# Performance work log

Hardware: AMD Instinct MI355X
Metric: run time of the kernel (lower is better)

Reference implementation:

```python
import jax, jax.numpy as jnp
import numpy as np

BIN_AGG = 16  # binAgg in source
K = 3         # forward-default im2col/col2im kernel size


def _im2col(x, k):
    # torch Im2Col (unfold), pad=0, stride=1, dilation=1
    B, C, H, W = x.shape
    oh, ow = H - k + 1, W - k + 1
    patches = [x[:, :, i:i + oh, j:j + ow] for i in range(k) for j in range(k)]
    cols = jnp.stack(patches, axis=2)            # [B, C, k*k, oh, ow]
    return cols.reshape(B, C * k * k, oh * ow)   # [B, C*k*k, L]


def _col2im(cols, k, H, W):
    # torch Col2Im (fold): overlap-add of patches back to [B, C, H, W]
    B, CK, L = cols.shape
    C = CK // (k * k)
    oh = H - k + 1
    cols = cols.reshape(B, C, k, k, oh, oh)
    img = jnp.zeros((B, C, H, W), cols.dtype)
    for i in range(k):
        for j in range(k):
            img = img.at[:, :, i:i + oh, j:j + oh].add(cols[:, :, i, j])
    return img


def bin_active(x):
    # sign(x) scaled by block-wise mean of |x| over blocks of 16 along last dim
    B, Kd, L = x.shape
    blocks = jnp.abs(x).reshape(B, Kd, L // BIN_AGG, BIN_AGG)
    scale = jnp.mean(blocks, axis=-1, keepdims=True)
    scale = jnp.broadcast_to(scale, blocks.shape).reshape(B, Kd, L)
    return scale * jnp.sign(x)


def setup_inputs() -> dict:
    key = jax.random.key(0)
    ks = jax.random.split(key, 5)
    B, Cin, Cout, H = 8, 64, 128, 130
    x = jax.random.normal(ks[0], (B, Cin, H, H), jnp.float32)
    gamma = 1.0 + 0.1 * jax.random.normal(ks[1], (Cin,), jnp.float32)
    beta = 0.1 * jax.random.normal(ks[2], (Cin,), jnp.float32)
    conv_w = 0.05 * jax.random.normal(ks[3], (Cout, Cin, 3, 3), jnp.float32)
    conv_b = 0.05 * jax.random.normal(ks[4], (Cout,), jnp.float32)
    return {"x": x, "gamma": gamma, "beta": beta, "conv_w": conv_w, "conv_b": conv_b}


def reference(x, gamma, beta, conv_w, conv_b):
    eps = 1e-4  # BatchNorm2d eps in source
    # BatchNorm2d (training-mode batch statistics, affine)
    mean = jnp.mean(x, axis=(0, 2, 3), keepdims=True)
    var = jnp.var(x, axis=(0, 2, 3), keepdims=True)
    xbn = (x - mean) * jax.lax.rsqrt(var + eps) * gamma[None, :, None, None] + beta[None, :, None, None]
    H = x.shape[2]
    cols = _im2col(xbn, K)          # [B, C*9, (H-2)^2]
    cols = bin_active(cols)         # block-mean binary quantization
    img = _col2im(cols, K, H, H)    # [B, C, H, W]
    y = jax.lax.conv_general_dilated(
        img, conv_w, window_strides=(1, 1), padding=((1, 1), (1, 1)),
        dimension_numbers=("NCHW", "OIHW", "NCHW"))
    y = y + conv_b[None, :, None, None]
    return jax.nn.relu(y)
```

## Files before the change

### kernel.cpp

```cpp
#include <hip/hip_runtime.h>
#include <math.h>

#define B_    8
#define CIN   64
#define COUT  128
#define H_    130
#define NPIX  (H_*H_)
#define NPX   (B_*NPIX)
#define IMW   132
#define SLABU 4608

typedef __attribute__((ext_vector_type(8))) short short8;
typedef __attribute__((ext_vector_type(4))) float f32x4;

__device__ __forceinline__ ushort f2bf(float f) {
    uint u = __builtin_bit_cast(uint, f);
    uint r = (u + 0x7FFFu + ((u >> 16) & 1u)) >> 16;
    return (ushort)r;
}

__global__ __launch_bounds__(256) void bn_stage1(
    const float* __restrict__ x, float* __restrict__ part)
{
    const int c = blockIdx.x, b = blockIdx.y, tid = threadIdx.x;
    const float4* p = (const float4*)(x + ((size_t)b*CIN + c)*NPIX);
    float s = 0.f, q = 0.f;
    for (int i = tid; i < NPIX/4; i += 256) {
        float4 v = p[i];
        s += v.x + v.y + v.z + v.w;
        q += v.x*v.x + v.y*v.y + v.z*v.z + v.w*v.w;
    }
    #pragma unroll
    for (int off = 32; off; off >>= 1) { s += __shfl_down(s, off); q += __shfl_down(q, off); }
    __shared__ float ss[4], qq[4];
    if ((tid & 63) == 0) { ss[tid >> 6] = s; qq[tid >> 6] = q; }
    __syncthreads();
    if (tid == 0) {
        s = ss[0] + ss[1] + ss[2] + ss[3];
        q = qq[0] + qq[1] + qq[2] + qq[3];
        part[(c*B_ + b)*2]     = s;
        part[(c*B_ + b)*2 + 1] = q;
    }
}

__global__ __launch_bounds__(256) void wprep_bn(
    const float* __restrict__ w, const float* __restrict__ part,
    const float* __restrict__ gamma, const float* __restrict__ beta,
    ushort* __restrict__ wT, float* __restrict__ abuf, float* __restrict__ bbuf)
{
    int i = blockIdx.x*256 + threadIdx.x;
    int co = i / 576, k = i - co*576;
    int dydx = k >> 6, ci = k & 63;
    wT[i] = f2bf(w[co*576 + ci*9 + dydx]);
    if (blockIdx.x == 0 && threadIdx.x < 64) {
        int c = threadIdx.x;
        float s = 0.f, q = 0.f;
        for (int b = 0; b < B_; ++b) { s += part[(c*B_+b)*2]; q += part[(c*B_+b)*2+1]; }
        float mean = s * (1.0f/135200.f);
        float var  = q * (1.0f/135200.f) - mean*mean;
        float a = gamma[c] / sqrtf(var + 1e-4f);
        abuf[c] = a;
        bbuf[c] = beta[c] - mean * a;
    }
}

__global__ __launch_bounds__(256) void binfold(
    const float* __restrict__ x, const float* __restrict__ abuf,
    const float* __restrict__ bbuf, ushort* __restrict__ img)
{
    __shared__ __align__(16) ushort tile[H_*18];
    __shared__ float absrow[4][132];
    __shared__ float wsum[4][24];
    const int yy = blockIdx.x, b = blockIdx.y, zg = blockIdx.z;
    const int tid = threadIdx.x, wv = tid >> 6, lane = tid & 63;
    const int cgBase = zg*2;
    uint* u0 = (uint*)(img + ((size_t)(b*IMW + yy)*2)*SLABU);

    if (yy == 0 || yy == IMW-1) {
        for (int i = tid; i < 1088; i += 256) {
            int xhh = i / 544, r = i - xhh*544, c = r >> 3, p = r & 7;
            u0[(size_t)xhh*(SLABU/2) + ((cgBase + (p>>2))*72 + c)*4 + (p&3)] = 0u;
        }
        return;
    }
    const int y = yy - 1;
    const float county = (float)min(min(y + 1, 3), H_ - y);

    const int ci0 = zg*16 + wv*4;
    float v0[4], v1[4], v2[4];
    #pragma unroll
    for (int it = 0; it < 4; ++it) {
        const int ci = ci0 + it;
        const float* row = x + (((size_t)b*CIN + ci)*H_ + y)*H_;
        const float a = abuf[ci], bb = bbuf[ci];
        v0[it] = a*row[lane]      + bb;
        v1[it] = a*row[lane + 64] + bb;
        v2[it] = (lane < 2) ? (a*row[lane + 128] + bb) : 0.f;
    }

    #pragma unroll
    for (int it = 0; it < 4; ++it) {
        const int cl = wv*4 + it;
        absrow[wv][lane]      = fabsf(v0[it]);
        absrow[wv][lane + 64] = fabsf(v1[it]);
        if (lane < 2) absrow[wv][lane + 128] = fabsf(v2[it]);
        asm volatile("s_waitcnt lgkmcnt(0)" ::: "memory");
        if (lane < 24) {
            int j = lane >> 3, bx = lane & 7;
            int s = j + bx*16;
            float acc = 0.f;
            #pragma unroll
            for (int t = 0; t < 16; ++t) acc += absrow[wv][s + t];
            wsum[wv][j*8 + bx] = acc;
        }
        asm volatile("s_waitcnt lgkmcnt(0)" ::: "memory");
        #pragma unroll
        for (int rep = 0; rep < 3; ++rep) {
            int xp = lane + rep*64;
            if (xp < H_) {
                float v = (rep == 0) ? v0[it] : (rep == 1) ? v1[it] : v2[it];
                float sgn = (v > 0.f) ? 1.f : ((v < 0.f) ? -1.f : 0.f);
                float sum = 0.f;
                #pragma unroll
                for (int j = 0; j < 3; ++j) {
                    int ox = xp - j;
                    if ((unsigned)ox < 128u) sum += wsum[wv][j*8 + (ox >> 4)];
                }
                tile[xp*18 + cl] = f2bf(sgn * county * sum * 0.0625f);
            }
        }
        asm volatile("s_waitcnt lgkmcnt(0)" ::: "memory");
    }
    __syncthreads();
    const uint* tU = (const uint*)tile;
    for (int i = tid; i < 1088; i += 256) {
        int xhh = i / 544, r = i - xhh*544, c = r >> 3, p = r & 7;
        int xx = xhh*65 + c;
        if (xx > 131) continue;
        uint v = 0u;
        if (xx != 0 && xx != 131) v = tU[(xx-1)*9 + p];
        u0[(size_t)xhh*(SLABU/2) + ((cgBase + (p>>2))*72 + c)*4 + (p&3)] = v;
    }
}

__global__ __launch_bounds__(256, 4) void conv_mfma(
    const ushort* __restrict__ img, const ushort* __restrict__ wT,
    const float* __restrict__ bias, float* __restrict__ out)
{
    __shared__ __align__(64) ushort sB[3*SLABU];
    const int xh = blockIdx.x, y = blockIdx.y, b = blockIdx.z;
    const int tid = threadIdx.x, lane = tid & 63, q = tid >> 6;
    const int l16 = lane & 15, quad = lane >> 4;

    {
        const size_t rowBase = ((size_t)(b*IMW + y)*2 + xh);
        #pragma unroll
        for (int t = 0; t < 7; ++t) {
            int k = q + 4*t;
            if (k < 27) {
                int dy = (int)((unsigned)k / 9u), j = k - dy*9;
                const ushort* gs = img + (rowBase + (size_t)dy*2)*SLABU + j*512 + lane*8;
                ushort* ls = sB + k*512;
                __builtin_amdgcn_global_load_lds(
                    (const __attribute__((address_space(1))) uint*)gs,
                    (__attribute__((address_space(3))) uint*)ls, 16, 0, 0);
            }
        }
    }
    __syncthreads();

    const ushort* wA = wT + (size_t)(q*32 + l16)*576 + quad*8;
    short8 aP[3][2];
    #pragma unroll
    for (int mt = 0; mt < 2; ++mt) {
        aP[0][mt] = *(const short8*)(wA + mt*16*576);
        aP[1][mt] = *(const short8*)(wA + mt*16*576 + 32);
    }
    int colB[5];
    #pragma unroll
    for (int nt = 0; nt < 5; ++nt)
        colB[nt] = min(nt*16 + l16, 64);

    f32x4 acc[2][5];
    #pragma unroll
    for (int mt = 0; mt < 2; ++mt)
        #pragma unroll
        for (int nt = 0; nt < 5; ++nt)
            acc[mt][nt] = (f32x4){0.f, 0.f, 0.f, 0.f};

    #pragma unroll
    for (int s = 0; s < 18; ++s) {
        if (s < 16) {
            #pragma unroll
            for (int mt = 0; mt < 2; ++mt)
                aP[(s+2)%3][mt] = *(const short8*)(wA + mt*16*576 + (s+2)*32);
        }
        const int dydx = s >> 1, h = s & 1;
        const int dy = dydx / 3, dx = dydx - dy*3;
        const int base = dy*SLABU + ((h*4 + quad)*72 + dx)*8;
        short8 bf[5];
        #pragma unroll
        for (int nt = 0; nt < 5; ++nt)
            bf[nt] = *(const short8*)(sB + base + colB[nt]*8);
        #pragma unroll
        for (int mt = 0; mt < 2; ++mt)
            #pragma unroll
            for (int nt = 0; nt < 5; ++nt)
                acc[mt][nt] = __builtin_amdgcn_mfma_f32_16x16x32_bf16(
                    aP[s%3][mt], bf[nt], acc[mt][nt], 0, 0, 0);
    }

    const size_t ob = (size_t)b*COUT*NPIX + (size_t)y*H_ + xh*65;
    #pragma unroll
    for (int mt = 0; mt < 2; ++mt) {
        #pragma unroll
        for (int r = 0; r < 4; ++r) {
            const int co = q*32 + mt*16 + quad*4 + r;
            const float bv = bias[co];
            #pragma unroll
            for (int nt = 0; nt < 5; ++nt) {
                int p = nt*16 + l16;
                if (p < 65) {
                    float v = acc[mt][nt][r] + bv;
                    out[ob + (size_t)co*NPIX + p] = v > 0.f ? v : 0.f;
                }
            }
        }
    }
}

extern "C" void kernel_launch(void* const* d_in, const int* in_sizes, int n_in,
                              void* d_out, int out_size, void* d_ws, size_t ws_size,
                              hipStream_t stream)
{
    const float* x      = (const float*)d_in[0];
    const float* gamma  = (const float*)d_in[1];
    const float* beta   = (const float*)d_in[2];
    const float* conv_w = (const float*)d_in[3];
    const float* conv_b = (const float*)d_in[4];
    float* out = (float*)d_out;

    float*  part = (float*)d_ws;
    float*  abuf = part + 1024;
    float*  bbuf = abuf + 64;
    ushort* wT   = (ushort*)(bbuf + 64);
    ushort* img  = wT + 73728;

    bn_stage1<<<dim3(CIN, B_), 256, 0, stream>>>(x, part);
    wprep_bn<<<288, 256, 0, stream>>>(conv_w, part, gamma, beta, wT, abuf, bbuf);
    binfold<<<dim3(IMW, B_, 4), 256, 0, stream>>>(x, abuf, bbuf, img);
    conv_mfma<<<dim3(2, H_, B_), 256, 0, stream>>>(img, wT, conv_b, out);
}
```

Measured before the change: 185.6 us.

## Fuse weight prep into BN stats, inline BN finalize, strip conv over 4 rows

Moves the weight bf16 transpose into the BN statistics kernel and recomputes the per-channel BN affine inside binfold, removing one kernel launch. The conv kernel now processes a strip of 4 output rows per block. It loads 6 image rows into LDS once and keeps all 36 weight fragments plus the bias in registers, reusing them across the rows. The cost is higher register and LDS use per block: the launch bound drops to 2 blocks per CU and the grid shrinks, which lowers occupancy and parallelism.

```diff
diff --git a/kernel.cpp b/kernel.cpp
--- a/kernel.cpp
+++ b/kernel.cpp
@@ -9,6 +9,7 @@
 #define NPX   (B_*NPIX)
 #define IMW   132
 #define SLABU 4608
+#define RSTRIP 4
 
 typedef __attribute__((ext_vector_type(8))) short short8;
 typedef __attribute__((ext_vector_type(4))) float f32x4;
@@ -19,10 +20,18 @@
     return (ushort)r;
 }
 
-__global__ __launch_bounds__(256) void bn_stage1(
-    const float* __restrict__ x, float* __restrict__ part)
+__global__ __launch_bounds__(256) void bnw_stage1(
+    const float* __restrict__ x, const float* __restrict__ w,
+    float* __restrict__ part, ushort* __restrict__ wT)
 {
     const int c = blockIdx.x, b = blockIdx.y, tid = threadIdx.x;
+    const int flat = b*64 + c;
+    if (flat < 288) {
+        int i = flat*256 + tid;
+        int co = i / 576, k = i - co*576;
+        int dydx = k >> 6, ci = k & 63;
+        wT[i] = f2bf(w[co*576 + ci*9 + dydx]);
+    }
     const float4* p = (const float4*)(x + ((size_t)b*CIN + c)*NPIX);
     float s = 0.f, q = 0.f;
     for (int i = tid; i < NPIX/4; i += 256) {
@@ -43,34 +52,15 @@
     }
 }
 
-__global__ __launch_bounds__(256) void wprep_bn(
-    const float* __restrict__ w, const float* __restrict__ part,
+__global__ __launch_bounds__(256) void binfold(
+    const float* __restrict__ x, const float* __restrict__ part,
     const float* __restrict__ gamma, const float* __restrict__ beta,
-    ushort* __restrict__ wT, float* __restrict__ abuf, float* __restrict__ bbuf)
-{
-    int i = blockIdx.x*256 + threadIdx.x;
-    int co = i / 576, k = i - co*576;
-    int dydx = k >> 6, ci = k & 63;
-    wT[i] = f2bf(w[co*576 + ci*9 + dydx]);
-    if (blockIdx.x == 0 && threadIdx.x < 64) {
-        int c = threadIdx.x;
-        float s = 0.f, q = 0.f;
-        for (int b = 0; b < B_; ++b) { s += part[(c*B_+b)*2]; q += part[(c*B_+b)*2+1]; }
-        float mean = s * (1.0f/135200.f);
-        float var  = q * (1.0f/135200.f) - mean*mean;
-        float a = gamma[c] / sqrtf(var + 1e-4f);
-        abuf[c] = a;
-        bbuf[c] = beta[c] - mean * a;
-    }
-}
-
-__global__ __launch_bounds__(256) void binfold(
-    const float* __restrict__ x, const float* __restrict__ abuf,
-    const float* __restrict__ bbuf, ushort* __restrict__ img)
+    ushort* __restrict__ img)
 {
     __shared__ __align__(16) ushort tile[H_*18];
     __shared__ float absrow[4][132];
     __shared__ float wsum[4][24];
+    __shared__ float sA[4][4], sBt[4][4];
     const int yy = blockIdx.x, b = blockIdx.y, zg = blockIdx.z;
     const int tid = threadIdx.x, wv = tid >> 6, lane = tid & 63;
     const int cgBase = zg*2;
@@ -87,12 +77,28 @@
     const float county = (float)min(min(y + 1, 3), H_ - y);
 
     const int ci0 = zg*16 + wv*4;
+    if (lane < 4) {
+        int ci = ci0 + lane;
+        float s = 0.f, q = 0.f;
+        #pragma unroll
+        for (int bb = 0; bb < B_; ++bb) {
+            s += part[(ci*B_ + bb)*2];
+            q += part[(ci*B_ + bb)*2 + 1];
+        }
+        float mean = s * (1.0f/135200.f);
+        float var  = q * (1.0f/135200.f) - mean*mean;
+        float a = gamma[ci] / sqrtf(var + 1e-4f);
+        sA[wv][lane]  = a;
+        sBt[wv][lane] = beta[ci] - mean * a;
+    }
+    asm volatile("s_waitcnt lgkmcnt(0)" ::: "memory");
+
     float v0[4], v1[4], v2[4];
     #pragma unroll
     for (int it = 0; it < 4; ++it) {
         const int ci = ci0 + it;
         const float* row = x + (((size_t)b*CIN + ci)*H_ + y)*H_;
-        const float a = abuf[ci], bb = bbuf[ci];
+        const float a = sA[wv][it], bb = sBt[wv][it];
         v0[it] = a*row[lane]      + bb;
         v1[it] = a*row[lane + 64] + bb;
         v2[it] = (lane < 2) ? (a*row[lane + 128] + bb) : 0.f;
@@ -143,86 +149,94 @@
     }
 }
 
-__global__ __launch_bounds__(256, 4) void conv_mfma(
+__global__ __launch_bounds__(256, 2) void conv_mfma(
     const ushort* __restrict__ img, const ushort* __restrict__ wT,
     const float* __restrict__ bias, float* __restrict__ out)
 {
-    __shared__ __align__(64) ushort sB[3*SLABU];
-    const int xh = blockIdx.x, y = blockIdx.y, b = blockIdx.z;
+    __shared__ __align__(64) ushort sB[6*SLABU];
+    const int xh = blockIdx.x, ys = blockIdx.y, b = blockIdx.z;
+    const int y0 = ys*RSTRIP;
     const int tid = threadIdx.x, lane = tid & 63, q = tid >> 6;
     const int l16 = lane & 15, quad = lane >> 4;
 
-    {
-        const size_t rowBase = ((size_t)(b*IMW + y)*2 + xh);
-        #pragma unroll
-        for (int t = 0; t < 7; ++t) {
-            int k = q + 4*t;
-            if (k < 27) {
-                int dy = (int)((unsigned)k / 9u), j = k - dy*9;
-                const ushort* gs = img + (rowBase + (size_t)dy*2)*SLABU + j*512 + lane*8;
-                ushort* ls = sB + k*512;
-                __builtin_amdgcn_global_load_lds(
-                    (const __attribute__((address_space(1))) uint*)gs,
-                    (__attribute__((address_space(3))) uint*)ls, 16, 0, 0);
-            }
-        }
-    }
-    __syncthreads();
+    #pragma unroll
+    for (int t = 0; t < 14; ++t) {
+        int k = q + 4*t;
+        if (k < 54) {
+            int sl = (int)((unsigned)k / 9u), j = k - sl*9;
+            int yy = min(y0 + sl, IMW-1);
+            const ushort* gs = img + ((size_t)(b*IMW + yy)*2 + xh)*SLABU
+                               + j*512 + lane*8;
+            __builtin_amdgcn_global_load_lds(
+                (const __attribute__((address_space(1))) uint*)gs,
+                (__attribute__((address_space(3))) uint*)(sB + k*512), 16, 0, 0);
+        }
+    }
 
     const ushort* wA = wT + (size_t)(q*32 + l16)*576 + quad*8;
-    short8 aP[3][2];
-    #pragma unroll
-    for (int mt = 0; mt < 2; ++mt) {
-        aP[0][mt] = *(const short8*)(wA + mt*16*576);
-        aP[1][mt] = *(const short8*)(wA + mt*16*576 + 32);
-    }
+    short8 aReg[36];
+    #pragma unroll
+    for (int mt = 0; mt < 2; ++mt)
+        #pragma unroll
+        for (int s = 0; s < 18; ++s)
+            aReg[mt*18 + s] = *(const short8*)(wA + mt*16*576 + s*32);
+
+    float bv[8];
+    #pragma unroll
+    for (int mt = 0; mt < 2; ++mt)
+        #pragma unroll
+        for (int rr = 0; rr < 4; ++rr)
+            bv[mt*4 + rr] = bias[q*32 + mt*16 + quad*4 + rr];
+
     int colB[5];
     #pragma unroll
     for (int nt = 0; nt < 5; ++nt)
         colB[nt] = min(nt*16 + l16, 64);
 
-    f32x4 acc[2][5];
-    #pragma unroll
-    for (int mt = 0; mt < 2; ++mt)
-        #pragma unroll
-        for (int nt = 0; nt < 5; ++nt)
-            acc[mt][nt] = (f32x4){0.f, 0.f, 0.f, 0.f};
-
-    #pragma unroll
-    for (int s = 0; s < 18; ++s) {
-        if (s < 16) {
+    __syncthreads();
+
+    #pragma unroll
+    for (int r = 0; r < RSTRIP; ++r) {
+        const int y = y0 + r;
+        if (y < H_) {
+            f32x4 acc[2][5];
             #pragma unroll
             for (int mt = 0; mt < 2; ++mt)
-                aP[(s+2)%3][mt] = *(const short8*)(wA + mt*16*576 + (s+2)*32);
-        }
-        const int dydx = s >> 1, h = s & 1;
-        const int dy = dydx / 3, dx = dydx - dy*3;
-        const int base = dy*SLABU + ((h*4 + quad)*72 + dx)*8;
-        short8 bf[5];
-        #pragma unroll
-        for (int nt = 0; nt < 5; ++nt)
-            bf[nt] = *(const short8*)(sB + base + colB[nt]*8);
-        #pragma unroll
-        for (int mt = 0; mt < 2; ++mt)
-            #pragma unroll
-            for (int nt = 0; nt < 5; ++nt)
-                acc[mt][nt] = __builtin_amdgcn_mfma_f32_16x16x32_bf16(
-                    aP[s%3][mt], bf[nt], acc[mt][nt], 0, 0, 0);
-    }
-
-    const size_t ob = (size_t)b*COUT*NPIX + (size_t)y*H_ + xh*65;
-    #pragma unroll
-    for (int mt = 0; mt < 2; ++mt) {
-        #pragma unroll
-        for (int r = 0; r < 4; ++r) {
-            const int co = q*32 + mt*16 + quad*4 + r;
-            const float bv = bias[co];
-            #pragma unroll
-            for (int nt = 0; nt < 5; ++nt) {
-                int p = nt*16 + l16;
-                if (p < 65) {
-                    float v = acc[mt][nt][r] + bv;
-                    out[ob + (size_t)co*NPIX + p] = v > 0.f ? v : 0.f;
+                #pragma unroll
+                for (int nt = 0; nt < 5; ++nt)
+                    acc[mt][nt] = (f32x4){0.f, 0.f, 0.f, 0.f};
+
+            #pragma unroll
+            for (int s = 0; s < 18; ++s) {
+                const int dydx = s >> 1, h = s & 1;
+                const int dy = dydx / 3, dx = dydx - dy*3;
+                const int base = (r + dy)*SLABU + ((h*4 + quad)*72 + dx)*8;
+                short8 bf[5];
+                #pragma unroll
+                for (int nt = 0; nt < 5; ++nt)
+                    bf[nt] = *(const short8*)(sB + base + colB[nt]*8);
+                #pragma unroll
+                for (int mt = 0; mt < 2; ++mt)
+                    #pragma unroll
+                    for (int nt = 0; nt < 5; ++nt)
+                        acc[mt][nt] = __builtin_amdgcn_mfma_f32_16x16x32_bf16(
+                            aReg[mt*18 + s], bf[nt], acc[mt][nt], 0, 0, 0);
+            }
+
+            const size_t ob = (size_t)b*COUT*NPIX + (size_t)y*H_ + xh*65;
+            #pragma unroll
+            for (int mt = 0; mt < 2; ++mt) {
+                #pragma unroll
+                for (int rr = 0; rr < 4; ++rr) {
+                    const int co = q*32 + mt*16 + quad*4 + rr;
+                    #pragma unroll
+                    for (int nt = 0; nt < 5; ++nt) {
+                        int p = nt*16 + l16;
+                        if (p < 65) {
+                            float v = acc[mt][nt][rr] + bv[mt*4 + rr];
+                            out[ob + (size_t)co*NPIX + p] = v > 0.f ? v : 0.f;
+                        }
+                    }
                 }
             }
         }
@@ -241,13 +255,10 @@
     float* out = (float*)d_out;
 
     float*  part = (float*)d_ws;
-    float*  abuf = part + 1024;
-    float*  bbuf = abuf + 64;
-    ushort* wT   = (ushort*)(bbuf + 64);
+    ushort* wT   = (ushort*)(part + 1024);
     ushort* img  = wT + 73728;
 
-    bn_stage1<<<dim3(CIN, B_), 256, 0, stream>>>(x, part);
-    wprep_bn<<<288, 256, 0, stream>>>(conv_w, part, gamma, beta, wT, abuf, bbuf);
-    binfold<<<dim3(IMW, B_, 4), 256, 0, stream>>>(x, abuf, bbuf, img);
-    conv_mfma<<<dim3(2, H_, B_), 256, 0, stream>>>(img, wT, conv_b, out);
-}
+    bnw_stage1<<<dim3(CIN, B_), 256, 0, stream>>>(x, conv_w, part, wT);
+    binfold<<<dim3(IMW, B_, 4), 256, 0, stream>>>(x, part, gamma, beta, img);
+    conv_mfma<<<dim3(2, (H_ + RSTRIP - 1)/RSTRIP, B_), 256, 0, stream>>>(img, wT, conv_b, out);
+}
```

New measurement: 167.3 us. 1.11x faster.
